# Kernel tuning notes

Measured on AMD Instinct MI355X. Metric: run time of the kernel, lower is better.

The kernel has to match this reference:

```python
import jax, jax.numpy as jnp
import numpy as np

N, C, E = 50000, 128, 800000
HEADS, S_TYPES = 4, 3
ATTN_DIM = 128
HEAD_DIM = ATTN_DIM // HEADS
LN_EPS = 1e-5


def setup_inputs() -> dict:
    key = jax.random.key(0)
    ks = jax.random.split(key, 12)
    sc = 1.0 / np.sqrt(C)
    return {
        "x": jax.random.normal(ks[0], (N, C), jnp.float32),
        "structure_type": jax.random.randint(ks[1], (N,), 0, S_TYPES),
        "edge_index": jax.random.randint(ks[2], (2, E), 0, N),
        "Wq": jax.random.normal(ks[3], (C, ATTN_DIM), jnp.float32) * sc,
        "bq": jnp.zeros((ATTN_DIM,), jnp.float32),
        "Wk": jax.random.normal(ks[4], (C, ATTN_DIM), jnp.float32) * sc,
        "bk": jnp.zeros((ATTN_DIM,), jnp.float32),
        "Wv": jax.random.normal(ks[5], (C, ATTN_DIM), jnp.float32) * sc,
        "bv": jnp.zeros((ATTN_DIM,), jnp.float32),
        "structure_bias": jnp.zeros((S_TYPES, HEADS), jnp.float32),
        "Wo": jax.random.normal(ks[6], (ATTN_DIM, C), jnp.float32) * sc,
        "bo": jnp.zeros((C,), jnp.float32),
        "ln_gamma": jnp.ones((C,), jnp.float32),
        "ln_beta": jnp.zeros((C,), jnp.float32),
    }


def reference(x, structure_type, edge_index, Wq, bq, Wk, bk, Wv, bv,
              structure_bias, Wo, bo, ln_gamma, ln_beta):
    residual = x
    q = (x @ Wq + bq).reshape(N, HEADS, HEAD_DIM)
    k = (x @ Wk + bk).reshape(N, HEADS, HEAD_DIM)
    v = (x @ Wv + bv).reshape(N, HEADS, HEAD_DIM)
    src, dst = edge_index[0], edge_index[1]
    # per-edge scores [E, H]
    attn = jnp.sum(q[dst] * k[src], axis=-1) / np.sqrt(HEAD_DIM)
    attn = attn + structure_bias[structure_type[src]]
    # segment softmax over dst
    m = jax.ops.segment_max(attn, dst, num_segments=N)  # [N, H]
    e = jnp.exp(attn - m[dst])
    s = jax.ops.segment_sum(e, dst, num_segments=N)     # [N, H]
    a = e / (s[dst] + 1e-16)
    # scatter-add messages -> [N, H, Hd]
    out = jax.ops.segment_sum(a[..., None] * v[src], dst, num_segments=N)
    out = out.reshape(N, ATTN_DIM) @ Wo + bo
    y = residual + out
    mu = jnp.mean(y, axis=-1, keepdims=True)
    var = jnp.var(y, axis=-1, keepdims=True)
    return (y - mu) / jnp.sqrt(var + LN_EPS) * ln_gamma + ln_beta
```

## Files before the change

### kernel.cpp

```cpp
#include <hip/hip_runtime.h>
#include <hip/hip_bf16.h>
#include <hip/hip_fp8.h>

#define HEADS 4
#define CDIM 128
#define INV_SQRT_HD 0.17677669529663687f
#define BCAP 64
#define KVROW 384
#define NBINS 256
#define BINCAP 6144
#define BIN_EPB 4096

using short8  = __attribute__((ext_vector_type(8))) short;
using float4v = __attribute__((ext_vector_type(4))) float;
using float2v = __attribute__((ext_vector_type(2))) float;
#if __has_builtin(__builtin_amdgcn_fdot2_f32_bf16)
using bf16x2 = __attribute__((ext_vector_type(2))) __bf16;
__device__ __forceinline__ bf16x2 asbf2(unsigned u) {
    return __builtin_bit_cast(bf16x2, u);
}
#endif

__device__ __forceinline__ float bflo(unsigned u) { return __uint_as_float(u << 16); }
__device__ __forceinline__ float bfhi(unsigned u) { return __uint_as_float(u & 0xffff0000u); }
__device__ __forceinline__ short bfr(float f) {
    __hip_bfloat16 h = __float2bfloat16(f);
    return *(short*)&h;
}

__global__ __launch_bounds__(256) void wswz_kernel(
    const float* __restrict__ Wq, const float* __restrict__ Wk,
    const float* __restrict__ Wv, const float* __restrict__ Wo,
    unsigned short* __restrict__ wt, int* __restrict__ gcur)
{
    int i = blockIdx.x * 256 + threadIdx.x;
    if (i < NBINS) gcur[i] = 0;
    if (i >= 4 * 16384) return;
    int m = i >> 14, rem = i & 16383;
    int col = rem & 127, k = rem >> 7;
    const float* W = (m == 0) ? Wq : (m == 1) ? Wk : (m == 2) ? Wv : Wo;
    wt[(m << 14) + col * 128 + k] = (unsigned short)bfr(W[k * 128 + col]);
}

__global__ __launch_bounds__(256) void qkv_bin_kernel(
    const float* __restrict__ x, const unsigned short* __restrict__ wt,
    const float* __restrict__ bq, const float* __restrict__ bk,
    const float* __restrict__ bv,
    unsigned short* __restrict__ q,
    unsigned char* __restrict__ kvb,
    int N,
    const int* __restrict__ ei, const int* __restrict__ stype,
    int* __restrict__ gcur, uint2* __restrict__ binned, int E,
    int binBlocks)
{
    __shared__ unsigned short wl[128 * 136];

    const int t = threadIdx.x;

    if ((int)blockIdx.x < binBlocks) {
        int* lcnt  = (int*)wl;
        int* lbase = lcnt + NBINS;
        const int base = (int)blockIdx.x * BIN_EPB;

        if (t < NBINS) lcnt[t] = 0;
        __syncthreads();

        int mybin[16], myloc[16];
        uint2 myent[16];
        #pragma unroll
        for (int j = 0; j < 16; ++j) {
            int i = base + j * 256 + t;
            mybin[j] = -1;
            if (i < E) {
                int src = ei[i];
                int dst = ei[E + i];
                int st  = stype[src];
                int bin = dst >> 8;
                mybin[j] = bin;
                myloc[j] = atomicAdd(&lcnt[bin], 1);
                myent[j] = make_uint2((unsigned)(src | (st << 16)), (unsigned)dst);
            }
        }
        __syncthreads();

        if (t < NBINS) lbase[t] = atomicAdd(&gcur[t], lcnt[t]);
        __syncthreads();

        #pragma unroll
        for (int j = 0; j < 16; ++j) {
            if (mybin[j] >= 0) {
                int pos = lbase[mybin[j]] + myloc[j];
                if (pos < BINCAP)
                    binned[(size_t)mybin[j] * BINCAP + pos] = myent[j];
            }
        }
        return;
    }

    const int lane = t & 63;
    const int w = t >> 6;
    const int n = lane & 15, qd = lane >> 4;
    const int rowb = ((int)blockIdx.x - binBlocks) * 64 + w * 16;

    int arow = rowb + n;
    int arowc = (arow < N) ? arow : (N - 1);
    const float4* x4 = (const float4*)(x + (size_t)arowc * 128);
    short8 afrag[4];
    #pragma unroll
    for (int c = 0; c < 4; ++c) {
        float4 f0 = x4[c * 8 + qd * 2];
        float4 f1 = x4[c * 8 + qd * 2 + 1];
        short8 a;
        a[0] = bfr(f0.x); a[1] = bfr(f0.y); a[2] = bfr(f0.z); a[3] = bfr(f0.w);
        a[4] = bfr(f1.x); a[5] = bfr(f1.y); a[6] = bfr(f1.z); a[7] = bfr(f1.w);
        afrag[c] = a;
    }

    for (int m = 0; m < 3; ++m) {
        __syncthreads();
        const uint4* g4 = (const uint4*)(wt + (m << 14));
        #pragma unroll
        for (int i = 0; i < 8; ++i) {
            int id = t + 256 * i;
            int col = id >> 4, ch = id & 15;
            *(uint4*)&wl[col * 136 + ch * 8] = g4[col * 16 + ch];
        }
        __syncthreads();

        float4v acc[8];
        #pragma unroll
        for (int tt = 0; tt < 8; ++tt) acc[tt] = (float4v){0.f, 0.f, 0.f, 0.f};

        #pragma unroll
        for (int c = 0; c < 4; ++c) {
            #pragma unroll
            for (int tt = 0; tt < 8; ++tt) {
                short8 bfrag = *(const short8*)&wl[(tt * 16 + n) * 136 + c * 32 + qd * 8];
                acc[tt] = __builtin_amdgcn_mfma_f32_16x16x32_bf16(
                    afrag[c], bfrag, acc[tt], 0, 0, 0);
            }
        }

        const float* bptr = (m == 0) ? bq : (m == 1) ? bk : bv;
        #pragma unroll
        for (int tt = 0; tt < 8; ++tt) {
            int gcol = tt * 16 + n;
            float bb = bptr[gcol];
            #pragma unroll
            for (int r = 0; r < 4; ++r) {
                int grow = rowb + qd * 4 + r;
                if (grow < N) {
                    float val = acc[tt][r] + bb;
                    if (m == 0) {
                        q[(size_t)grow * 128 + gcol] = (unsigned short)bfr(val);
                    } else if (m == 1) {
                        *(unsigned short*)(kvb + (size_t)grow * KVROW + gcol * 2)
                            = (unsigned short)bfr(val);
                    } else {
                        __hip_fp8_e4m3 f8(val);
                        kvb[(size_t)grow * KVROW + 256 + gcol] = f8.__x;
                    }
                }
            }
        }
    }
}

__global__ __launch_bounds__(1024) void bucket_kernel(
    const uint2* __restrict__ binned, const int* __restrict__ gcur,
    int* __restrict__ buckets, int* __restrict__ cnt, int N)
{
    __shared__ int lcnt[256];
    const int t = threadIdx.x;
    const int bin = blockIdx.x;

    if (t < 256) lcnt[t] = 0;
    __syncthreads();

    int ne = gcur[bin];
    ne = (ne < BINCAP) ? ne : BINCAP;
    const uint2* brow = binned + (size_t)bin * BINCAP;

    for (int i = t; i < ne; i += 1024) {
        uint2 e = brow[i];
        int dst = (int)e.y;
        int pos = atomicAdd(&lcnt[dst & 255], 1);
        if (pos < BCAP) buckets[(size_t)dst * BCAP + pos] = (int)e.x;
    }
    __syncthreads();

    if (t < 256) {
        int dst = bin * 256 + t;
        if (dst < N) {
            int c = lcnt[t];
            cnt[dst] = (c < BCAP) ? c : BCAP;
        }
    }
}

__global__ __launch_bounds__(256) void attn_csr_kernel(
    const unsigned short* __restrict__ q,
    const unsigned char* __restrict__ kv,
    const int* __restrict__ cnt, const int* __restrict__ buckets,
    const float* __restrict__ sbias,
    unsigned short* __restrict__ h,
    int N)
{
    int wid = (blockIdx.x * 256 + threadIdx.x) >> 6;
    if (wid >= N) return;
    int lane = threadIdx.x & 63;
    int qt = lane >> 4;
    int ql = lane & 15;
    int hd = ql >> 2;

    float sb0 = sbias[hd];
    float sb1 = sbias[HEADS + hd];
    float sb2 = sbias[2 * HEADS + hd];

    int d = cnt[wid];
    d = (d < BCAP) ? d : BCAP;
    const int* brow = buckets + (size_t)wid * BCAP;

    const uint4* qrow = (const uint4*)(q + (size_t)wid * 128);
    uint4 qu = qrow[ql];
#if !__has_builtin(__builtin_amdgcn_fdot2_f32_bf16)
    float2v qp0 = {bflo(qu.x), bfhi(qu.x)};
    float2v qp1 = {bflo(qu.y), bfhi(qu.y)};
    float2v qp2 = {bflo(qu.z), bfhi(qu.z)};
    float2v qp3 = {bflo(qu.w), bfhi(qu.w)};
#endif

    if (d == 0) {
        if (qt == 0) {
            uint4 z = make_uint4(0, 0, 0, 0);
            *(uint4*)(h + (size_t)wid * 128 + ql * 8) = z;
        }
        return;
    }

    int ent = (lane < d) ? brow[lane] : 0;

    float2v a01 = {0.f, 0.f}, a23 = {0.f, 0.f};
    float2v a45 = {0.f, 0.f}, a67 = {0.f, 0.f};
    float sacc = 0.f;

    int nit = (d + 3) >> 2;
    int i0 = qt;

    int ic0 = (i0 < d) ? i0 : (d - 1);
    int se0 = __shfl(ent, ic0);
    const unsigned char* kp0 = kv + (size_t)(se0 & 0xffff) * KVROW;
    uint4 ku0 = *(const uint4*)(kp0 + ql * 16);
    uint2 vu0 = *(const uint2*)(kp0 + 256 + ql * 8);

    int se1 = se0; uint4 ku1 = ku0; uint2 vu1 = vu0;
    if (nit > 1) {
        int i1 = i0 + 4;
        int ic1 = (i1 < d) ? i1 : (d - 1);
        se1 = __shfl(ent, ic1);
        const unsigned char* kp1 = kv + (size_t)(se1 & 0xffff) * KVROW;
        ku1 = *(const uint4*)(kp1 + ql * 16);
        vu1 = *(const uint2*)(kp1 + 256 + ql * 8);
    }

    for (int it = 0; it < nit; ++it) {
        int se2 = se1; uint4 ku2 = ku1; uint2 vu2 = vu1;
        if (it + 2 < nit) {
            int i2 = i0 + 8;
            int ic2 = (i2 < d) ? i2 : (d - 1);
            se2 = __shfl(ent, ic2);
            const unsigned char* kp2 = kv + (size_t)(se2 & 0xffff) * KVROW;
            ku2 = *(const uint4*)(kp2 + ql * 16);
            vu2 = *(const uint2*)(kp2 + 256 + ql * 8);
        }

#if __has_builtin(__builtin_amdgcn_fdot2_f32_bf16)
        float p;
        p = __builtin_amdgcn_fdot2_f32_bf16(asbf2(ku0.x), asbf2(qu.x), 0.f, false);
        p = __builtin_amdgcn_fdot2_f32_bf16(asbf2(ku0.y), asbf2(qu.y), p, false);
        p = __builtin_amdgcn_fdot2_f32_bf16(asbf2(ku0.z), asbf2(qu.z), p, false);
        p = __builtin_amdgcn_fdot2_f32_bf16(asbf2(ku0.w), asbf2(qu.w), p, false);
#else
        float2v k01 = {bflo(ku0.x), bfhi(ku0.x)};
        float2v k23 = {bflo(ku0.y), bfhi(ku0.y)};
        float2v k45 = {bflo(ku0.z), bfhi(ku0.z)};
        float2v k67 = {bflo(ku0.w), bfhi(ku0.w)};
        float2v pp = k01 * qp0;
        pp += k23 * qp1;
        pp += k45 * qp2;
        pp += k67 * qp3;
        float p = pp.x + pp.y;
#endif
        p += __shfl_xor(p, 1);
        p += __shfl_xor(p, 2);

        int st = se0 >> 16;
        float bias = (st == 0) ? sb0 : ((st == 1) ? sb1 : sb2);
        float ev = __expf(fmaf(p, INV_SQRT_HD, bias));
        ev = (i0 < d) ? ev : 0.f;
        float2v ev2 = {ev, ev};

#if __has_builtin(__builtin_amdgcn_cvt_pk_f32_fp8)
        a01 += ev2 * __builtin_amdgcn_cvt_pk_f32_fp8(vu0.x, false);
        a23 += ev2 * __builtin_amdgcn_cvt_pk_f32_fp8(vu0.x, true);
        a45 += ev2 * __builtin_amdgcn_cvt_pk_f32_fp8(vu0.y, false);
        a67 += ev2 * __builtin_amdgcn_cvt_pk_f32_fp8(vu0.y, true);
#else
        a01.x = fmaf(ev, __builtin_amdgcn_cvt_f32_fp8(vu0.x, 0), a01.x);
        a01.y = fmaf(ev, __builtin_amdgcn_cvt_f32_fp8(vu0.x, 1), a01.y);
        a23.x = fmaf(ev, __builtin_amdgcn_cvt_f32_fp8(vu0.x, 2), a23.x);
        a23.y = fmaf(ev, __builtin_amdgcn_cvt_f32_fp8(vu0.x, 3), a23.y);
        a45.x = fmaf(ev, __builtin_amdgcn_cvt_f32_fp8(vu0.y, 0), a45.x);
        a45.y = fmaf(ev, __builtin_amdgcn_cvt_f32_fp8(vu0.y, 1), a45.y);
        a67.x = fmaf(ev, __builtin_amdgcn_cvt_f32_fp8(vu0.y, 2), a67.x);
        a67.y = fmaf(ev, __builtin_amdgcn_cvt_f32_fp8(vu0.y, 3), a67.y);
#endif
        sacc += ev;

        se0 = se1; ku0 = ku1; vu0 = vu1;
        se1 = se2; ku1 = ku2; vu1 = vu2;
        i0 += 4;
    }

    float accs[8] = {a01.x, a01.y, a23.x, a23.y, a45.x, a45.y, a67.x, a67.y};
    #pragma unroll
    for (int j = 0; j < 8; ++j) {
        accs[j] += __shfl_xor(accs[j], 16);
        accs[j] += __shfl_xor(accs[j], 32);
    }
    sacc += __shfl_xor(sacc, 16);
    sacc += __shfl_xor(sacc, 32);

    if (qt == 0) {
        float inv = 1.0f / (sacc + 1e-16f);
        unsigned hw[4];
        #pragma unroll
        for (int j = 0; j < 4; ++j) {
            unsigned lo = (unsigned)(unsigned short)bfr(accs[2 * j] * inv);
            unsigned hi = (unsigned)(unsigned short)bfr(accs[2 * j + 1] * inv);
            hw[j] = lo | (hi << 16);
        }
        *(uint4*)(h + (size_t)wid * 128 + ql * 8) = *(uint4*)hw;
    }
}

__global__ __launch_bounds__(256) void out_ln_mfma_kernel(
    const unsigned short* __restrict__ hbuf, const unsigned short* __restrict__ wt,
    const float* __restrict__ bo, const float* __restrict__ x,
    const float* __restrict__ gamma, const float* __restrict__ beta,
    float* __restrict__ out, int N)
{
    __shared__ unsigned short wl[128 * 136];

    const int t = threadIdx.x;
    const int lane = t & 63;
    const int w = t >> 6;
    const int n = lane & 15, qd = lane >> 4;
    const int rowb = blockIdx.x * 64 + w * 16;

    const uint4* g4 = (const uint4*)(wt + (3 << 14));
    #pragma unroll
    for (int i = 0; i < 8; ++i) {
        int id = t + 256 * i;
        int col = id >> 4, ch = id & 15;
        *(uint4*)&wl[col * 136 + ch * 8] = g4[col * 16 + ch];
    }

    int arow = rowb + n;
    int arowc = (arow < N) ? arow : (N - 1);
    const unsigned short* hrow = hbuf + (size_t)arowc * 128;
    short8 afrag[4];
    #pragma unroll
    for (int c = 0; c < 4; ++c)
        afrag[c] = *(const short8*)(hrow + c * 32 + qd * 8);
    __syncthreads();

    float4v acc[8];
    #pragma unroll
    for (int tt = 0; tt < 8; ++tt) acc[tt] = (float4v){0.f, 0.f, 0.f, 0.f};

    #pragma unroll
    for (int c = 0; c < 4; ++c) {
        #pragma unroll
        for (int tt = 0; tt < 8; ++tt) {
            short8 bfrag = *(const short8*)&wl[(tt * 16 + n) * 136 + c * 32 + qd * 8];
            acc[tt] = __builtin_amdgcn_mfma_f32_16x16x32_bf16(
                afrag[c], bfrag, acc[tt], 0, 0, 0);
        }
    }

    float bov[8];
    #pragma unroll
    for (int tt = 0; tt < 8; ++tt) bov[tt] = bo[tt * 16 + n];

    float sum[4], sq[4];
    #pragma unroll
    for (int r = 0; r < 4; ++r) {
        int grow = rowb + qd * 4 + r;
        int growc = (grow < N) ? grow : (N - 1);
        const float* xr = x + (size_t)growc * 128;
        float s = 0.f, s2 = 0.f;
        #pragma unroll
        for (int tt = 0; tt < 8; ++tt) {
            float yv = acc[tt][r] + bov[tt] + xr[tt * 16 + n];
            acc[tt][r] = yv;
            s += yv;
            s2 += yv * yv;
        }
        sum[r] = s; sq[r] = s2;
    }
    #pragma unroll
    for (int off = 1; off < 16; off <<= 1) {
        #pragma unroll
        for (int r = 0; r < 4; ++r) {
            sum[r] += __shfl_xor(sum[r], off);
            sq[r]  += __shfl_xor(sq[r], off);
        }
    }

    float gv[8], bv2[8];
    #pragma unroll
    for (int tt = 0; tt < 8; ++tt) { gv[tt] = gamma[tt * 16 + n]; bv2[tt] = beta[tt * 16 + n]; }

    #pragma unroll
    for (int r = 0; r < 4; ++r) {
        int grow = rowb + qd * 4 + r;
        if (grow >= N) continue;
        float mu   = sum[r] * (1.0f / 128.0f);
        float var  = sq[r] * (1.0f / 128.0f) - mu * mu;
        float rstd = rsqrtf(var + 1e-5f);
        float* orow = out + (size_t)grow * 128;
        #pragma unroll
        for (int tt = 0; tt < 8; ++tt)
            orow[tt * 16 + n] = (acc[tt][r] - mu) * rstd * gv[tt] + bv2[tt];
    }
}

extern "C" void kernel_launch(void* const* d_in, const int* in_sizes, int n_in,
                              void* d_out, int out_size, void* d_ws, size_t ws_size,
                              hipStream_t stream) {
    const float* x     = (const float*)d_in[0];
    const int*   stype = (const int*)  d_in[1];
    const int*   ei    = (const int*)  d_in[2];
    const float* Wq    = (const float*)d_in[3];
    const float* bq    = (const float*)d_in[4];
    const float* Wk    = (const float*)d_in[5];
    const float* bk    = (const float*)d_in[6];
    const float* Wv    = (const float*)d_in[7];
    const float* bv    = (const float*)d_in[8];
    const float* sbias = (const float*)d_in[9];
    const float* Wo    = (const float*)d_in[10];
    const float* bo    = (const float*)d_in[11];
    const float* gam   = (const float*)d_in[12];
    const float* bet   = (const float*)d_in[13];
    float* out = (float*)d_out;

    const int N = in_sizes[0] / CDIM;
    const int E = in_sizes[2] / 2;

    char* wsb = (char*)d_ws;
    unsigned short* q       = (unsigned short*)wsb;
    unsigned short* h       = (unsigned short*)(wsb + (size_t)N * 256);
    unsigned char*  kvb     = (unsigned char*)(wsb + (size_t)N * 512);
    int*            buckets = (int*)(wsb + (size_t)N * 896);
    int*            cnt     = (int*)(wsb + (size_t)N * 1152);
    size_t gcur_off = (size_t)N * 1152 + (((size_t)N * 4 + 255) & ~(size_t)255);
    int*            gcur    = (int*)(wsb + gcur_off);
    uint2*          binned  = (uint2*)(wsb + gcur_off + 1024);
    unsigned short* wt      = (unsigned short*)(wsb + gcur_off + 1024
                                  + (size_t)NBINS * BINCAP * 8);

    dim3 blk(256);

    const int qkvBlocks = (N + 63) / 64;
    const int binBlocks = (E + BIN_EPB - 1) / BIN_EPB;

    wswz_kernel<<<dim3(256), blk, 0, stream>>>(Wq, Wk, Wv, Wo, wt, gcur);

    qkv_bin_kernel<<<dim3(qkvBlocks + binBlocks), blk, 0, stream>>>(
        x, wt, bq, bk, bv, q, kvb, N, ei, stype, gcur, binned, E, binBlocks);

    bucket_kernel<<<dim3(NBINS), dim3(1024), 0, stream>>>(
        binned, gcur, buckets, cnt, N);

    attn_csr_kernel<<<dim3((N * 64 + 255) / 256), blk, 0, stream>>>(
        q, kvb, cnt, buckets, sbias, h, N);

    out_ln_mfma_kernel<<<dim3((N + 63) / 64), blk, 0, stream>>>(
        h, wt, bo, x, gam, bet, out, N);
}
```

Measured before the change: 202.1 us.

## Regroup preprocessing: fuse binning with weight swizzle, bucketing with QKV projection

Restructures the preprocessing stages so that edge binning runs in the same launch as the weight transpose/bf16 conversion, and per-destination bucketing runs in the same launch as the QKV MFMA projection. The gcur reset moves to a hipMemsetAsync. The goal is fewer dependent kernel launches and letting the small bucket pass overlap with the compute-bound projection. The bucket pass now uses 256 threads per bin instead of 1024, and the memset adds a separate stream operation.

```diff
diff --git a/kernel.cpp b/kernel.cpp
--- a/kernel.cpp
+++ b/kernel.cpp
@@ -28,38 +28,19 @@
     return *(short*)&h;
 }
 
-__global__ __launch_bounds__(256) void wswz_kernel(
+__global__ __launch_bounds__(256) void wswz_bin_kernel(
     const float* __restrict__ Wq, const float* __restrict__ Wk,
     const float* __restrict__ Wv, const float* __restrict__ Wo,
-    unsigned short* __restrict__ wt, int* __restrict__ gcur)
-{
-    int i = blockIdx.x * 256 + threadIdx.x;
-    if (i < NBINS) gcur[i] = 0;
-    if (i >= 4 * 16384) return;
-    int m = i >> 14, rem = i & 16383;
-    int col = rem & 127, k = rem >> 7;
-    const float* W = (m == 0) ? Wq : (m == 1) ? Wk : (m == 2) ? Wv : Wo;
-    wt[(m << 14) + col * 128 + k] = (unsigned short)bfr(W[k * 128 + col]);
-}
-
-__global__ __launch_bounds__(256) void qkv_bin_kernel(
-    const float* __restrict__ x, const unsigned short* __restrict__ wt,
-    const float* __restrict__ bq, const float* __restrict__ bk,
-    const float* __restrict__ bv,
-    unsigned short* __restrict__ q,
-    unsigned char* __restrict__ kvb,
-    int N,
+    unsigned short* __restrict__ wt,
     const int* __restrict__ ei, const int* __restrict__ stype,
     int* __restrict__ gcur, uint2* __restrict__ binned, int E,
     int binBlocks)
 {
-    __shared__ unsigned short wl[128 * 136];
-
+    __shared__ int lcnt[NBINS];
+    __shared__ int lbase[NBINS];
     const int t = threadIdx.x;
 
     if ((int)blockIdx.x < binBlocks) {
-        int* lcnt  = (int*)wl;
-        int* lbase = lcnt + NBINS;
         const int base = (int)blockIdx.x * BIN_EPB;
 
         if (t < NBINS) lcnt[t] = 0;
@@ -97,10 +78,59 @@
         return;
     }
 
+    int i = ((int)blockIdx.x - binBlocks) * 256 + t;
+    if (i >= 4 * 16384) return;
+    int m = i >> 14, rem = i & 16383;
+    int col = rem & 127, k = rem >> 7;
+    const float* W = (m == 0) ? Wq : (m == 1) ? Wk : (m == 2) ? Wv : Wo;
+    wt[(m << 14) + col * 128 + k] = (unsigned short)bfr(W[k * 128 + col]);
+}
+
+__global__ __launch_bounds__(256) void qkv_bucket_kernel(
+    const float* __restrict__ x, const unsigned short* __restrict__ wt,
+    const float* __restrict__ bq, const float* __restrict__ bk,
+    const float* __restrict__ bv,
+    unsigned short* __restrict__ q,
+    unsigned char* __restrict__ kvb,
+    int N,
+    const uint2* __restrict__ binned, const int* __restrict__ gcur,
+    int* __restrict__ buckets, int* __restrict__ cnt)
+{
+    __shared__ unsigned short wl[128 * 136];
+
+    const int t = threadIdx.x;
+
+    if ((int)blockIdx.x < NBINS) {
+        int* lcnt = (int*)wl;
+        const int bin = blockIdx.x;
+
+        lcnt[t] = 0;
+        __syncthreads();
+
+        int ne = gcur[bin];
+        ne = (ne < BINCAP) ? ne : BINCAP;
+        const uint2* brow = binned + (size_t)bin * BINCAP;
+
+        for (int i = t; i < ne; i += 256) {
+            uint2 e = brow[i];
+            int dst = (int)e.y;
+            int pos = atomicAdd(&lcnt[dst & 255], 1);
+            if (pos < BCAP) buckets[(size_t)dst * BCAP + pos] = (int)e.x;
+        }
+        __syncthreads();
+
+        int dst = bin * 256 + t;
+        if (dst < N) {
+            int c = lcnt[t];
+            cnt[dst] = (c < BCAP) ? c : BCAP;
+        }
+        return;
+    }
+
     const int lane = t & 63;
     const int w = t >> 6;
     const int n = lane & 15, qd = lane >> 4;
-    const int rowb = ((int)blockIdx.x - binBlocks) * 64 + w * 16;
+    const int rowb = ((int)blockIdx.x - NBINS) * 64 + w * 16;
 
     int arow = rowb + n;
     int arowc = (arow < N) ? arow : (N - 1);
@@ -166,38 +196,6 @@
     }
 }
 
-__global__ __launch_bounds__(1024) void bucket_kernel(
-    const uint2* __restrict__ binned, const int* __restrict__ gcur,
-    int* __restrict__ buckets, int* __restrict__ cnt, int N)
-{
-    __shared__ int lcnt[256];
-    const int t = threadIdx.x;
-    const int bin = blockIdx.x;
-
-    if (t < 256) lcnt[t] = 0;
-    __syncthreads();
-
-    int ne = gcur[bin];
-    ne = (ne < BINCAP) ? ne : BINCAP;
-    const uint2* brow = binned + (size_t)bin * BINCAP;
-
-    for (int i = t; i < ne; i += 1024) {
-        uint2 e = brow[i];
-        int dst = (int)e.y;
-        int pos = atomicAdd(&lcnt[dst & 255], 1);
-        if (pos < BCAP) buckets[(size_t)dst * BCAP + pos] = (int)e.x;
-    }
-    __syncthreads();
-
-    if (t < 256) {
-        int dst = bin * 256 + t;
-        if (dst < N) {
-            int c = lcnt[t];
-            cnt[dst] = (c < BCAP) ? c : BCAP;
-        }
-    }
-}
-
 __global__ __launch_bounds__(256) void attn_csr_kernel(
     const unsigned short* __restrict__ q,
     const unsigned char* __restrict__ kv,
@@ -475,13 +473,13 @@
     const int qkvBlocks = (N + 63) / 64;
     const int binBlocks = (E + BIN_EPB - 1) / BIN_EPB;
 
-    wswz_kernel<<<dim3(256), blk, 0, stream>>>(Wq, Wk, Wv, Wo, wt, gcur);
-
-    qkv_bin_kernel<<<dim3(qkvBlocks + binBlocks), blk, 0, stream>>>(
-        x, wt, bq, bk, bv, q, kvb, N, ei, stype, gcur, binned, E, binBlocks);
-
-    bucket_kernel<<<dim3(NBINS), dim3(1024), 0, stream>>>(
-        binned, gcur, buckets, cnt, N);
+    hipMemsetAsync(gcur, 0, NBINS * sizeof(int), stream);
+
+    wswz_bin_kernel<<<dim3(binBlocks + 256), blk, 0, stream>>>(
+        Wq, Wk, Wv, Wo, wt, ei, stype, gcur, binned, E, binBlocks);
+
+    qkv_bucket_kernel<<<dim3(NBINS + qkvBlocks), blk, 0, stream>>>(
+        x, wt, bq, bk, bv, q, kvb, N, binned, gcur, buckets, cnt);
 
     attn_csr_kernel<<<dim3((N * 64 + 255) / 256), blk, 0, stream>>>(
         q, kvb, cnt, buckets, sbias, h, N);
```

After: 209.4 us. 3.6% more time.
